# Kernel tuning notes

Measured on AMD Instinct MI355X. Metric: run time of the kernel, lower is better.

The kernel has to match this reference:

```python
import jax, jax.numpy as jnp
import numpy as np

D_EMB = 768
N_HEADS = 12
D_K = D_EMB // N_HEADS


def setup_inputs() -> dict:
    key = jax.random.key(0)
    k0, k1, k2, k3, k4 = jax.random.split(key, 5)
    B, S = 2, 4096
    scale = 1.0 / np.sqrt(D_EMB)
    return {
        "inputs": jax.random.normal(k0, (B, S, D_EMB), dtype=jnp.float32),
        "Wq": jax.random.normal(k1, (D_EMB, D_EMB), dtype=jnp.float32) * scale,
        "Wk": jax.random.normal(k2, (D_EMB, D_EMB), dtype=jnp.float32) * scale,
        "Wv": jax.random.normal(k3, (D_EMB, D_EMB), dtype=jnp.float32) * scale,
        "Wo": jax.random.normal(k4, (D_EMB, D_EMB), dtype=jnp.float32) * scale,
    }


def reference(inputs, Wq, Wk, Wv, Wo):
    B, S, _ = inputs.shape
    def split_heads(x):  # [B,S,E] -> [B,H,S,dk]
        return x.reshape(B, S, N_HEADS, D_K).transpose(0, 2, 1, 3)
    q = split_heads(inputs @ Wq)
    k = split_heads(inputs @ Wk)
    v = split_heads(inputs @ Wv)
    scores = jnp.einsum("bhqd,bhkd->bhqk", q, k) / jnp.sqrt(
        jnp.asarray(D_K, dtype=inputs.dtype)
    )
    attn = jax.nn.softmax(scores, axis=-1)
    out = jnp.einsum("bhqk,bhkd->bhqd", attn, v)
    out = out.transpose(0, 2, 1, 3).reshape(B, S, D_EMB)
    return out @ Wo
```

## Files before the change

kernel.cpp:

```cpp
#include <hip/hip_runtime.h>

#define D_EMB 768
#define NH 12
#define DK 64
#define NB 2
#define SS 4096
#define E3 (3*D_EMB)
#define MM (NB*SS)

typedef unsigned short u16;
typedef __attribute__((ext_vector_type(8))) __bf16 bf16x8;
typedef __attribute__((ext_vector_type(4))) float f32x4;
typedef __attribute__((ext_vector_type(4))) unsigned int u32x4;

static __device__ __forceinline__ u16 f2bf(float f) {
  unsigned u = __builtin_bit_cast(unsigned, f);
  u += 0x7fffu + ((u >> 16) & 1u);
  return (u16)(u >> 16);
}
static __device__ __forceinline__ f32x4 mfma16(bf16x8 a, bf16x8 b, f32x4 c) {
  return __builtin_amdgcn_mfma_f32_16x16x32_bf16(a, b, c, 0, 0, 0);
}
static __device__ __forceinline__ float exp2_fast(float x) {
#if __has_builtin(__builtin_amdgcn_exp2f)
  return __builtin_amdgcn_exp2f(x);
#else
  return __builtin_exp2f(x);
#endif
}
static __device__ __forceinline__ float rcp_fast(float x) {
#if __has_builtin(__builtin_amdgcn_rcpf)
  return __builtin_amdgcn_rcpf(x);
#else
  return 1.f / x;
#endif
}
static __device__ __forceinline__ void gload_lds16(const u16* g, u16* l) {
  __builtin_amdgcn_global_load_lds((const __attribute__((address_space(1))) void*)g,
                                   (__attribute__((address_space(3))) void*)l, 16, 0, 0);
}

__global__ __launch_bounds__(256) void cast_kernel(const float* __restrict__ in,
                                                   u16* __restrict__ out, int n) {
  int i = (blockIdx.x * 256 + threadIdx.x) * 4;
  if (i + 3 < n) {
    float4 v = *(const float4*)(in + i);
    out[i + 0] = f2bf(v.x);
    out[i + 1] = f2bf(v.y);
    out[i + 2] = f2bf(v.z);
    out[i + 3] = f2bf(v.w);
  }
}

__global__ __launch_bounds__(256) void transpose_cast_all(const float* __restrict__ Wq,
                                                          const float* __restrict__ Wk,
                                                          const float* __restrict__ Wv,
                                                          const float* __restrict__ Wo,
                                                          u16* __restrict__ WTqkv,
                                                          u16* __restrict__ WoT, float qscale) {
  __shared__ float tile[32][33];
  int z = blockIdx.z;
  const float* W = (z == 0) ? Wq : (z == 1) ? Wk : (z == 2) ? Wv : Wo;
  u16* WT = (z < 3) ? WTqkv + (size_t)z * D_EMB * D_EMB : WoT;
  float scale = (z == 0) ? qscale : 1.0f;
  int kb = blockIdx.y * 32, nb = blockIdx.x * 32;
  int tx = threadIdx.x, ty = threadIdx.y;
#pragma unroll
  for (int i = 0; i < 4; i++)
    tile[ty + i * 8][tx] = W[(size_t)(kb + ty + i * 8) * D_EMB + nb + tx];
  __syncthreads();
#pragma unroll
  for (int i = 0; i < 4; i++)
    WT[(size_t)(nb + ty + i * 8) * D_EMB + kb + tx] = f2bf(tile[tx][ty + i * 8] * scale);
}

__global__ __launch_bounds__(256) void transpose_v(const u16* __restrict__ QKV,
                                                   u16* __restrict__ VT) {
  __shared__ u16 tile[32][33];
  int bh = blockIdx.z;
  int b = bh / NH, h = bh % NH;
  int sb = blockIdx.x * 32, db = blockIdx.y * 32;
  int tx = threadIdx.x, ty = threadIdx.y;
  const u16* src = QKV + (size_t)(b * SS) * E3 + 2 * D_EMB + h * DK;
  u16* dst = VT + (size_t)bh * DK * SS;
#pragma unroll
  for (int i = 0; i < 4; i++)
    tile[ty + i * 8][tx] = src[(size_t)(sb + ty + i * 8) * E3 + db + tx];
  __syncthreads();
  int s = sb + tx;
  int k6 = s & 63;
  int p = (s & ~63) | (k6 & 0x23) | ((k6 & 0x0C) << 1) | ((k6 & 0x10) >> 2);
#pragma unroll
  for (int i = 0; i < 4; i++)
    dst[(size_t)(db + ty + i * 8) * SS + p] = tile[tx][ty + i * 8];
}

template <int OUTF32>
__global__ __launch_bounds__(256) void gemm_bt(const u16* __restrict__ A,
                                               const u16* __restrict__ Bt,
                                               void* __restrict__ Cout,
                                               int M, int N, int K, float scale) {
  __shared__ __align__(16) u16 As[128 * 32];
  __shared__ __align__(16) u16 Bs[128 * 32];
  int tid = threadIdx.x;
  int wave = tid >> 6, lane = tid & 63;
  int g = lane >> 4, nIdx = lane & 15;
  int m0 = blockIdx.y * 128, n0 = blockIdx.x * 128;
  int wm = (wave >> 1) * 64, wn = (wave & 1) * 64;

  f32x4 acc[4][4] = {};

  int row = tid >> 2, co = (tid & 3) * 8;
  int row2 = row + 64;

  for (int k0 = 0; k0 < K; k0 += 32) {
    __syncthreads();
    gload_lds16(A  + (size_t)(m0 + row)  * K + k0 + co, As + row  * 32 + co);
    gload_lds16(Bt + (size_t)(n0 + row)  * K + k0 + co, Bs + row  * 32 + co);
    gload_lds16(A  + (size_t)(m0 + row2) * K + k0 + co, As + row2 * 32 + co);
    gload_lds16(Bt + (size_t)(n0 + row2) * K + k0 + co, Bs + row2 * 32 + co);
    __syncthreads();

    bf16x8 af[4], bfr[4];
#pragma unroll
    for (int i = 0; i < 4; i++)
      af[i] = *(const bf16x8*)(As + (wm + i * 16 + nIdx) * 32 + g * 8);
#pragma unroll
    for (int j = 0; j < 4; j++)
      bfr[j] = *(const bf16x8*)(Bs + (wn + j * 16 + nIdx) * 32 + g * 8);
#pragma unroll
    for (int i = 0; i < 4; i++)
#pragma unroll
      for (int j = 0; j < 4; j++)
        acc[i][j] = mfma16(af[i], bfr[j], acc[i][j]);
  }

#pragma unroll
  for (int i = 0; i < 4; i++)
#pragma unroll
    for (int j = 0; j < 4; j++)
#pragma unroll
      for (int r = 0; r < 4; r++) {
        int rr = m0 + wm + i * 16 + g * 4 + r;
        int cc = n0 + wn + j * 16 + nIdx;
        float v = acc[i][j][r] * scale;
        if (OUTF32)
          ((float*)Cout)[(size_t)rr * N + cc] = v;
        else
          ((u16*)Cout)[(size_t)rr * N + cc] = f2bf(v);
      }
}

__global__ __launch_bounds__(256, 2) void flash(const u16* __restrict__ QKV,
                                                const u16* __restrict__ VT,
                                                u16* __restrict__ O) {
  __shared__ __align__(16) u16 smem[18432];

  int b = blockIdx.z, h = blockIdx.y;
  int q0 = blockIdx.x * 128;
  int tid = threadIdx.x, w = tid >> 6, l = tid & 63;
  int g = l >> 4, n = l & 15;
  int qh = w & 1, st = w >> 1;

  const u16* VTb = VT + (size_t)(b * NH + h) * DK * SS;
  u16* pKs = smem + st * 9216;
  u16* pVs = pKs + 4608;

  const u16* Qbase = QKV + (size_t)(b * SS + q0 + qh * 64) * E3 + h * DK;
  bf16x8 qf[4][2];
#pragma unroll
  for (int qg = 0; qg < 4; qg++)
#pragma unroll
    for (int hf = 0; hf < 2; hf++)
      qf[qg][hf] = *(const bf16x8*)(Qbase + (size_t)(qg * 16 + n) * E3 + hf * 32 + g * 8);

  f32x4 o_acc[4][4] = {};
  float lsum[4] = {0.f, 0.f, 0.f, 0.f};
  u32x4 onev = {0x3F803F80u, 0x3F803F80u, 0x3F803F80u, 0x3F803F80u};
  bf16x8 aone = __builtin_bit_cast(bf16x8, onev);

  int rL = l >> 3, cL = l & 7;
  const u16* g0;
  size_t rstep, tstep;
  u16* sW;
  if ((w & 1) == 0) {
    g0 = QKV + ((size_t)(b * SS) + st * 2048 + rL) * E3 + D_EMB + h * DK + cL * 8;
    rstep = (size_t)8 * E3;
    tstep = (size_t)64 * E3;
    sW = pKs + rL * 72 + cL * 8;
  } else {
    g0 = VTb + (size_t)rL * SS + st * 2048 + cL * 8;
    rstep = (size_t)8 * SS;
    tstep = 64;
    sW = pVs + rL * 72 + cL * 8;
  }

  for (int kt = 0; kt < 32; kt++) {
    __syncthreads();
    {
      const u16* gn = g0 + (size_t)kt * tstep;
      uint4 t[8];
#pragma unroll
      for (int i = 0; i < 8; i++)
        t[i] = *(const uint4*)(gn + i * rstep);
#pragma unroll
      for (int i = 0; i < 8; i++)
        *(uint4*)(sW + i * 576) = t[i];
    }
    __syncthreads();

#pragma unroll
    for (int s = 0; s < 2; s++) {
      bf16x8 kf[2][2];
#pragma unroll
      for (int jj = 0; jj < 2; jj++)
#pragma unroll
        for (int hf = 0; hf < 2; hf++)
          kf[jj][hf] = *(const bf16x8*)(pKs + ((2 * s + jj) * 16 + n) * 72 + hf * 32 + g * 8);

#pragma unroll
      for (int p = 0; p < 2; p++) {
        f32x4 C[2][2];
#pragma unroll
        for (int q2 = 0; q2 < 2; q2++) {
          int qg = 2 * p + q2;
#pragma unroll
          for (int jj = 0; jj < 2; jj++) {
            f32x4 t = {};
            t = mfma16(kf[jj][0], qf[qg][0], t);
            t = mfma16(kf[jj][1], qf[qg][1], t);
            C[q2][jj] = t;
          }
        }
        u32x4 Bw[2];
#pragma unroll
        for (int q2 = 0; q2 < 2; q2++)
#pragma unroll
          for (int jj = 0; jj < 2; jj++) {
            float p0 = exp2_fast(C[q2][jj][0]);
            float p1 = exp2_fast(C[q2][jj][1]);
            float p2 = exp2_fast(C[q2][jj][2]);
            float p3 = exp2_fast(C[q2][jj][3]);
            Bw[q2][jj * 2] = __builtin_amdgcn_perm(__builtin_bit_cast(unsigned, p1),
                                                   __builtin_bit_cast(unsigned, p0), 0x07060302u);
            Bw[q2][jj * 2 + 1] = __builtin_amdgcn_perm(__builtin_bit_cast(unsigned, p3),
                                                       __builtin_bit_cast(unsigned, p2), 0x07060302u);
          }
#pragma unroll
        for (int q2 = 0; q2 < 2; q2++) {
          f32x4 z = {};
          z = mfma16(aone, __builtin_bit_cast(bf16x8, Bw[q2]), z);
          lsum[2 * p + q2] += z[0];
        }
#pragma unroll
        for (int dt = 0; dt < 4; dt++) {
          bf16x8 vf = *(const bf16x8*)(pVs + (dt * 16 + n) * 72 + s * 32 + g * 8);
#pragma unroll
          for (int q2 = 0; q2 < 2; q2++)
            o_acc[2 * p + q2][dt] = mfma16(vf, __builtin_bit_cast(bf16x8, Bw[q2]),
                                           o_acc[2 * p + q2][dt]);
        }
      }
    }
  }

  __syncthreads();

  float* dumpF = (float*)smem;
  if (w >= 2) {
    float* dst = dumpF + ((size_t)((w - 2) * 64 + l)) * 68;
#pragma unroll
    for (int qg = 0; qg < 4; qg++)
#pragma unroll
      for (int dt = 0; dt < 4; dt++)
        *(f32x4*)(dst + (qg * 4 + dt) * 4) = o_acc[qg][dt];
    f32x4 lv = {lsum[0], lsum[1], lsum[2], lsum[3]};
    *(f32x4*)(dst + 64) = lv;
  }
  __syncthreads();
  if (w < 2) {
    float* src = dumpF + ((size_t)(w * 64 + l)) * 68;
#pragma unroll
    for (int qg = 0; qg < 4; qg++)
#pragma unroll
      for (int dt = 0; dt < 4; dt++)
        o_acc[qg][dt] += *(f32x4*)(src + (qg * 4 + dt) * 4);
    f32x4 lv = *(f32x4*)(src + 64);
#pragma unroll
    for (int qg = 0; qg < 4; qg++) {
      float rl = rcp_fast(lsum[qg] + lv[qg]);
      u16* Obp = O + (size_t)(b * SS + q0 + w * 64 + qg * 16 + n) * D_EMB + h * DK;
#pragma unroll
      for (int dt = 0; dt < 4; dt++) {
        uint2 pk;
        pk.x = (unsigned)f2bf(o_acc[qg][dt][0] * rl) |
               ((unsigned)f2bf(o_acc[qg][dt][1] * rl) << 16);
        pk.y = (unsigned)f2bf(o_acc[qg][dt][2] * rl) |
               ((unsigned)f2bf(o_acc[qg][dt][3] * rl) << 16);
        *(uint2*)(Obp + dt * 16 + g * 4) = pk;
      }
    }
  }
}

extern "C" void kernel_launch(void* const* d_in, const int* in_sizes, int n_in,
                              void* d_out, int out_size, void* d_ws, size_t ws_size,
                              hipStream_t stream) {
  const float* X  = (const float*)d_in[0];
  const float* Wq = (const float*)d_in[1];
  const float* Wk = (const float*)d_in[2];
  const float* Wv = (const float*)d_in[3];
  const float* Wo = (const float*)d_in[4];
  float* out = (float*)d_out;

  u16* Xb    = (u16*)d_ws;
  u16* WTqkv = Xb + (size_t)MM * D_EMB;
  u16* WoT   = WTqkv + (size_t)E3 * D_EMB;
  u16* QKV   = WoT + (size_t)D_EMB * D_EMB;
  u16* VT    = QKV + (size_t)MM * E3;
  u16* Ob    = VT + (size_t)NB * NH * DK * SS;

  dim3 tb(32, 8);
  cast_kernel<<<(MM * D_EMB) / 1024, 256, 0, stream>>>(X, Xb, MM * D_EMB);
  transpose_cast_all<<<dim3(24, 24, 4), tb, 0, stream>>>(Wq, Wk, Wv, Wo, WTqkv, WoT,
                                                         0.125f * 1.4426950408889634f);
  gemm_bt<0><<<dim3(E3 / 128, MM / 128), 256, 0, stream>>>(Xb, WTqkv, (void*)QKV,
                                                           MM, E3, D_EMB, 1.0f);
  transpose_v<<<dim3(SS / 32, 2, NB * NH), tb, 0, stream>>>(QKV, VT);
  flash<<<dim3(SS / 128, NH, NB), 256, 0, stream>>>(QKV, VT, Ob);
  gemm_bt<1><<<dim3(D_EMB / 128, MM / 128), 256, 0, stream>>>(Ob, WoT, (void*)out,
                                                              MM, D_EMB, D_EMB, 1.0f);
}
```

Before: 293.6 us.

## Double-buffer K/V tiles with async global-to-LDS loads and XOR swizzle

The flash kernel now prefetches the next K and V tile directly into a second LDS buffer with direct global-to-LDS loads while the current tile is being computed. This removes the register staging and one barrier per iteration. The padded row stride of 72 is replaced by an XOR-swizzled stride of 64 to avoid LDS bank conflicts. LDS use per block rises to 64KB, and correctness relies on the async loads finishing before the barrier at the top of each iteration.

After: 260.0 us. 11.4% less time.

```diff
diff --git a/kernel.cpp b/kernel.cpp
--- a/kernel.cpp
+++ b/kernel.cpp
@@ -154,7 +154,7 @@
 __global__ __launch_bounds__(256, 2) void flash(const u16* __restrict__ QKV,
                                                 const u16* __restrict__ VT,
                                                 u16* __restrict__ O) {
-  __shared__ __align__(16) u16 smem[18432];
+  __shared__ __align__(16) u16 smem[32768];
 
   int b = blockIdx.z, h = blockIdx.y;
   int q0 = blockIdx.x * 128;
@@ -163,8 +163,7 @@
   int qh = w & 1, st = w >> 1;
 
   const u16* VTb = VT + (size_t)(b * NH + h) * DK * SS;
-  u16* pKs = smem + st * 9216;
-  u16* pVs = pKs + 4608;
+  u16* sbase = smem + st * 16384;
 
   const u16* Qbase = QKV + (size_t)(b * SS + q0 + qh * 64) * E3 + h * DK;
   bf16x8 qf[4][2];
@@ -180,34 +179,40 @@
   bf16x8 aone = __builtin_bit_cast(bf16x8, onev);
 
   int rL = l >> 3, cL = l & 7;
+  int xr8 = (cL ^ rL) * 8;
   const u16* g0;
   size_t rstep, tstep;
-  u16* sW;
+  u16* sd0;
   if ((w & 1) == 0) {
-    g0 = QKV + ((size_t)(b * SS) + st * 2048 + rL) * E3 + D_EMB + h * DK + cL * 8;
+    g0 = QKV + ((size_t)(b * SS) + st * 2048 + rL) * E3 + D_EMB + h * DK + xr8;
     rstep = (size_t)8 * E3;
     tstep = (size_t)64 * E3;
-    sW = pKs + rL * 72 + cL * 8;
+    sd0 = sbase + l * 8;
   } else {
-    g0 = VTb + (size_t)rL * SS + st * 2048 + cL * 8;
+    g0 = VTb + (size_t)rL * SS + st * 2048 + xr8;
     rstep = (size_t)8 * SS;
     tstep = 64;
-    sW = pVs + rL * 72 + cL * 8;
-  }
-
+    sd0 = sbase + 4096 + l * 8;
+  }
+
+#pragma unroll
+  for (int i = 0; i < 8; i++)
+    gload_lds16(g0 + i * rstep, sd0 + i * 512);
+
+  int xrn = (n & 7);
   for (int kt = 0; kt < 32; kt++) {
     __syncthreads();
-    {
-      const u16* gn = g0 + (size_t)kt * tstep;
-      uint4 t[8];
+
+    const u16* pK = sbase + (kt & 1) * 8192;
+    const u16* pV = pK + 4096;
+
+    if (kt < 31) {
+      const u16* gn = g0 + (size_t)(kt + 1) * tstep;
+      u16* sd = sd0 + ((kt + 1) & 1) * 8192;
 #pragma unroll
       for (int i = 0; i < 8; i++)
-        t[i] = *(const uint4*)(gn + i * rstep);
-#pragma unroll
-      for (int i = 0; i < 8; i++)
-        *(uint4*)(sW + i * 576) = t[i];
+        gload_lds16(gn + i * rstep, sd + i * 512);
     }
-    __syncthreads();
 
 #pragma unroll
     for (int s = 0; s < 2; s++) {
@@ -216,7 +221,8 @@
       for (int jj = 0; jj < 2; jj++)
 #pragma unroll
         for (int hf = 0; hf < 2; hf++)
-          kf[jj][hf] = *(const bf16x8*)(pKs + ((2 * s + jj) * 16 + n) * 72 + hf * 32 + g * 8);
+          kf[jj][hf] = *(const bf16x8*)(pK + ((2 * s + jj) * 16 + n) * 64 +
+                                        ((hf * 4 + g) ^ xrn) * 8);
 
 #pragma unroll
       for (int p = 0; p < 2; p++) {
@@ -254,7 +260,8 @@
         }
 #pragma unroll
         for (int dt = 0; dt < 4; dt++) {
-          bf16x8 vf = *(const bf16x8*)(pVs + (dt * 16 + n) * 72 + s * 32 + g * 8);
+          bf16x8 vf = *(const bf16x8*)(pV + (dt * 16 + n) * 64 +
+                                       ((s * 4 + g) ^ xrn) * 8);
 #pragma unroll
           for (int q2 = 0; q2 < 2; q2++)
             o_acc[2 * p + q2][dt] = mfma16(vf, __builtin_bit_cast(bf16x8, Bw[q2]),
```
